# Kernel tuning notes

Measured on AMD Instinct MI355X. Metric: run time of the kernel, lower is better.

Reference implementation:

```python
import jax, jax.numpy as jnp
import numpy as np

VOCAB, HIDDEN, EMB_DIM = 30522, 768, 128
B, QLEN, DLEN = 1024, 32, 180
NEG = -1e4  # masked doc-token similarity
EPS = 1e-12


def setup_inputs() -> dict:
    key = jax.random.key(0)
    k1, k2, k3, k4, k5, k6 = jax.random.split(key, 6)
    return {
        "query_input_ids": jax.random.randint(k1, (B, QLEN), 0, VOCAB, dtype=jnp.int64) if jax.config.jax_enable_x64 else jax.random.randint(k1, (B, QLEN), 0, VOCAB, dtype=jnp.int32),
        "query_attention_mask": jax.random.randint(k2, (B, QLEN), 0, 2, dtype=jnp.int32),
        "doc_input_ids": jax.random.randint(k3, (B, DLEN), 0, VOCAB, dtype=jnp.int32),
        "doc_attention_mask": jax.random.randint(k4, (B, DLEN), 0, 2, dtype=jnp.int32),
        "embed_table": jax.random.normal(k5, (VOCAB, HIDDEN), dtype=jnp.float32) * 0.02,
        "proj_w": jax.random.normal(k6, (HIDDEN, EMB_DIM), dtype=jnp.float32) * 0.02,
        "proj_b": jnp.zeros((EMB_DIM,), dtype=jnp.float32),
    }


def _encode(ids, embed_table, proj_w, proj_b):
    # token embedding lookup -> linear projection -> L2 normalize (ColBERT-style)
    h = embed_table[ids]                      # (B, L, HIDDEN)
    e = jnp.einsum('blh,hd->bld', h, proj_w) + proj_b  # (B, L, EMB_DIM)
    e = e / (jnp.linalg.norm(e, axis=-1, keepdims=True) + EPS)
    return e


def reference(query_input_ids, query_attention_mask, doc_input_ids,
              doc_attention_mask, embed_table, proj_w, proj_b):
    q = _encode(query_input_ids, embed_table, proj_w, proj_b)  # (B, Q, D)
    d = _encode(doc_input_ids, embed_table, proj_w, proj_b)    # (B, T, D)
    # Batched MaxSim: sim[b,q,t] = <q_emb, d_emb>
    sim = jnp.einsum('bqd,btd->bqt', q, d)
    sim = jnp.where(doc_attention_mask[:, None, :] > 0, sim, NEG)
    max_sim = sim.max(axis=-1)                                  # (B, Q)
    scores = (max_sim * query_attention_mask.astype(max_sim.dtype)).sum(axis=-1)
    return scores  # (B,)
```

## Files before the change

kernel.cpp:

```cpp
#include <hip/hip_runtime.h>
#include <math.h>

#define VOCAB  30522
#define HIDDEN 768
#define EMB    128
#define BATCH  1024
#define QLEN   32
#define DLEN   180
#define NEGV   (-1e4f)

typedef __attribute__((ext_vector_type(8))) short bf16x8;
typedef __attribute__((ext_vector_type(4))) float f32x4;

__device__ __forceinline__ unsigned short f2bf(float x) {
  union { float f; unsigned u; } v; v.f = x;
  unsigned r = v.u + 0x7FFFu + ((v.u >> 16) & 1u);
  return (unsigned short)(r >> 16);
}
__device__ __forceinline__ float bf2f(unsigned short h) {
  union { float f; unsigned u; } v; v.u = ((unsigned)h) << 16;
  return v.f;
}

__global__ __launch_bounds__(256) void prep_wt(
    const float* __restrict__ W, unsigned short* __restrict__ wth,
    unsigned short* __restrict__ wtl) {
  __shared__ float tile[32][33];
  const int k0 = blockIdx.x * 32, n0 = blockIdx.y * 32;
  const int t = threadIdx.x, r = t >> 5, c = t & 31;
#pragma unroll
  for (int i = 0; i < 4; ++i) {
    int kr = r + i * 8;
    tile[kr][c] = W[(size_t)(k0 + kr) * EMB + n0 + c];
  }
  __syncthreads();
#pragma unroll
  for (int i = 0; i < 4; ++i) {
    int nr = r + i * 8;
    float x = tile[c][nr];
    unsigned short hi = f2bf(x);
    unsigned short lo = f2bf(x - bf2f(hi));
    wth[(size_t)(n0 + nr) * HIDDEN + k0 + c] = hi;
    wtl[(size_t)(n0 + nr) * HIDDEN + k0 + c] = lo;
  }
}

__global__ __launch_bounds__(256) void colbert_proj_mfma(
    const float* __restrict__ emb, const unsigned short* __restrict__ wth,
    const unsigned short* __restrict__ wtl, const float* __restrict__ bias,
    unsigned short* __restrict__ pebf) {
  __shared__ __align__(16) char smem[55296];
  unsigned short* Ah = (unsigned short*)smem;
  unsigned short* Al = Ah + 64 * 72;
  unsigned short* Wh = Al + 64 * 72;
  unsigned short* Wl = Wh + 128 * 72;

  const int tid  = threadIdx.x;
  const int lane = tid & 63;
  const int wid  = tid >> 6;
  const int wm   = wid & 1;
  const int wn   = wid >> 1;
  const int lr   = lane & 15;
  const int kq   = lane >> 4;
  const int row0 = blockIdx.x * 64;

  f32x4 acc[2][4];
#pragma unroll
  for (int mi = 0; mi < 2; ++mi)
#pragma unroll
    for (int ni = 0; ni < 4; ++ni) acc[mi][ni] = (f32x4)0.f;

  for (int hc = 0; hc < HIDDEN / 64; ++hc) {
    __syncthreads();
#pragma unroll
    for (int i = 0; i < 4; ++i) {
      int idx = i * 256 + tid;
      int row = idx >> 4, c4 = idx & 15;
      int gr = row0 + row; if (gr > VOCAB - 1) gr = VOCAB - 1;
      float4 v = *(const float4*)(emb + (size_t)gr * HIDDEN + hc * 64 + c4 * 4);
      float xs[4] = {v.x, v.y, v.z, v.w};
      ushort4 hh, ll;
      unsigned short* hp = (unsigned short*)&hh;
      unsigned short* lp = (unsigned short*)&ll;
#pragma unroll
      for (int j = 0; j < 4; ++j) {
        hp[j] = f2bf(xs[j]);
        lp[j] = f2bf(xs[j] - bf2f(hp[j]));
      }
      *(ushort4*)&Ah[row * 72 + c4 * 4] = hh;
      *(ushort4*)&Al[row * 72 + c4 * 4] = ll;
    }
#pragma unroll
    for (int i = 0; i < 4; ++i) {
      int idx = i * 256 + tid;
      int n = idx >> 3, k8 = idx & 7;
      size_t src = (size_t)n * HIDDEN + hc * 64 + k8 * 8;
      *(uint4*)&Wh[n * 72 + k8 * 8] = *(const uint4*)(wth + src);
      *(uint4*)&Wl[n * 72 + k8 * 8] = *(const uint4*)(wtl + src);
    }
    __syncthreads();

#pragma unroll
    for (int kk = 0; kk < 2; ++kk) {
      const int ko = kk * 32 + kq * 8;
      bf16x8 ah[2], al[2], bh[4], bl[4];
#pragma unroll
      for (int mi = 0; mi < 2; ++mi) {
        int r = wm * 32 + mi * 16 + lr;
        ah[mi] = *(bf16x8*)&Ah[r * 72 + ko];
        al[mi] = *(bf16x8*)&Al[r * 72 + ko];
      }
#pragma unroll
      for (int ni = 0; ni < 4; ++ni) {
        int n = wn * 64 + ni * 16 + lr;
        bh[ni] = *(bf16x8*)&Wh[n * 72 + ko];
        bl[ni] = *(bf16x8*)&Wl[n * 72 + ko];
      }
#pragma unroll
      for (int mi = 0; mi < 2; ++mi)
#pragma unroll
        for (int ni = 0; ni < 4; ++ni) {
          acc[mi][ni] = __builtin_amdgcn_mfma_f32_16x16x32_bf16(ah[mi], bh[ni], acc[mi][ni], 0, 0, 0);
          acc[mi][ni] = __builtin_amdgcn_mfma_f32_16x16x32_bf16(ah[mi], bl[ni], acc[mi][ni], 0, 0, 0);
          acc[mi][ni] = __builtin_amdgcn_mfma_f32_16x16x32_bf16(al[mi], bh[ni], acc[mi][ni], 0, 0, 0);
        }
    }
  }

  __syncthreads();
  float* ep = (float*)smem;
#pragma unroll
  for (int ni = 0; ni < 4; ++ni) {
    int col = wn * 64 + ni * 16 + lr;
    float bb = bias[col];
#pragma unroll
    for (int mi = 0; mi < 2; ++mi)
#pragma unroll
      for (int j = 0; j < 4; ++j) {
        int r = wm * 32 + mi * 16 + kq * 4 + j;
        ep[r * 132 + col] = acc[mi][ni][j] + bb;
      }
  }
  __syncthreads();
  {
    int row = tid >> 2, quad = tid & 3;
    float4 vv[8];
    float ss = 0.f;
#pragma unroll
    for (int i = 0; i < 8; ++i) {
      vv[i] = *(float4*)&ep[row * 132 + quad * 32 + i * 4];
      ss += vv[i].x * vv[i].x + vv[i].y * vv[i].y + vv[i].z * vv[i].z + vv[i].w * vv[i].w;
    }
    ss += __shfl_xor(ss, 1);
    ss += __shfl_xor(ss, 2);
    float sc = 1.f / (sqrtf(ss) + 1e-12f);
    int gr = row0 + row;
    if (gr < VOCAB) {
#pragma unroll
      for (int i = 0; i < 8; ++i) {
        ushort4 o;
        o.x = f2bf(vv[i].x * sc); o.y = f2bf(vv[i].y * sc);
        o.z = f2bf(vv[i].z * sc); o.w = f2bf(vv[i].w * sc);
        *(ushort4*)&pebf[(size_t)gr * EMB + quad * 32 + i * 4] = o;
      }
    }
  }
}

__global__ __launch_bounds__(256) void colbert_score_mfma(
    const int* __restrict__ qids, const int* __restrict__ qmask,
    const int* __restrict__ dids, const int* __restrict__ dmask,
    const unsigned short* __restrict__ pebf, float* __restrict__ out) {
  __shared__ int sqid[32];
  __shared__ int sdid[192];
  __shared__ unsigned char smsk[192];
  __shared__ float wmax[4][32];

  const int b    = blockIdx.x;
  const int tid  = threadIdx.x;
  const int lane = tid & 63;
  const int wid  = tid >> 6;
  const int lr   = lane & 15;
  const int kq   = lane >> 4;

  if (tid < 32) sqid[tid] = qids[b * QLEN + tid];
  if (tid < 192) {
    if (tid < DLEN) {
      sdid[tid] = dids[b * DLEN + tid];
      smsk[tid] = (unsigned char)(dmask[b * DLEN + tid] > 0 ? 1 : 0);
    } else {
      sdid[tid] = 0;
      smsk[tid] = 0;
    }
  }
  __syncthreads();

  bf16x8 af[2][4];
#pragma unroll
  for (int mi = 0; mi < 2; ++mi) {
    size_t base = (size_t)sqid[mi * 16 + lr] * EMB + kq * 8;
#pragma unroll
    for (int ks = 0; ks < 4; ++ks)
      af[mi][ks] = *(const bf16x8*)(pebf + base + ks * 32);
  }
  const int n0 = wid * 48;
  bf16x8 bf[3][4];
#pragma unroll
  for (int ni = 0; ni < 3; ++ni) {
    size_t base = (size_t)sdid[n0 + ni * 16 + lr] * EMB + kq * 8;
#pragma unroll
    for (int ks = 0; ks < 4; ++ks)
      bf[ni][ks] = *(const bf16x8*)(pebf + base + ks * 32);
  }

  f32x4 acc[2][3];
#pragma unroll
  for (int mi = 0; mi < 2; ++mi)
#pragma unroll
    for (int ni = 0; ni < 3; ++ni) acc[mi][ni] = (f32x4)0.f;

#pragma unroll
  for (int ks = 0; ks < 4; ++ks)
#pragma unroll
    for (int mi = 0; mi < 2; ++mi)
#pragma unroll
      for (int ni = 0; ni < 3; ++ni)
        acc[mi][ni] = __builtin_amdgcn_mfma_f32_16x16x32_bf16(af[mi][ks], bf[ni][ks], acc[mi][ni], 0, 0, 0);

#pragma unroll
  for (int mi = 0; mi < 2; ++mi) {
#pragma unroll
    for (int j = 0; j < 4; ++j) {
      float m = -3.0e38f;
#pragma unroll
      for (int ni = 0; ni < 3; ++ni) {
        int t = n0 + ni * 16 + lr;
        float s = smsk[t] ? acc[mi][ni][j] : NEGV;
        m = fmaxf(m, s);
      }
#pragma unroll
      for (int x = 1; x < 16; x <<= 1) m = fmaxf(m, __shfl_xor(m, x));
      if (lr == 0) wmax[wid][mi * 16 + kq * 4 + j] = m;
    }
  }
  __syncthreads();

  if (tid < 32) {
    float m = fmaxf(fmaxf(wmax[0][tid], wmax[1][tid]),
                    fmaxf(wmax[2][tid], wmax[3][tid]));
    float s = m * (float)qmask[b * QLEN + tid];
#pragma unroll
    for (int x = 1; x < 32; x <<= 1) s += __shfl_xor(s, x);
    if (tid == 0) out[b] = s;
  }
}

extern "C" void kernel_launch(void* const* d_in, const int* in_sizes, int n_in,
                              void* d_out, int out_size, void* d_ws, size_t ws_size,
                              hipStream_t stream) {
  const int*   qids  = (const int*)d_in[0];
  const int*   qmask = (const int*)d_in[1];
  const int*   dids  = (const int*)d_in[2];
  const int*   dmask = (const int*)d_in[3];
  const float* emb   = (const float*)d_in[4];
  const float* W     = (const float*)d_in[5];
  const float* bias  = (const float*)d_in[6];
  float*       out   = (float*)d_out;

  char* ws = (char*)d_ws;
  unsigned short* pebf = (unsigned short*)ws;
  unsigned short* wth  = (unsigned short*)(ws + 7813632);
  unsigned short* wtl  = (unsigned short*)(ws + 7813632 + 196608);

  prep_wt<<<dim3(HIDDEN / 32, EMB / 32), 256, 0, stream>>>(W, wth, wtl);
  colbert_proj_mfma<<<(VOCAB + 63) / 64, 256, 0, stream>>>(emb, wth, wtl, bias, pebf);
  colbert_score_mfma<<<BATCH, 256, 0, stream>>>(qids, qmask, dids, dmask, pebf, out);
}
```

Before: 51.03 us.

## Prepack W into MFMA fragment layout and double-buffer swizzled A tiles

The weight prep kernel now writes hi/lo bf16 splits of W directly in per-lane MFMA fragment order, so the projection kernel loads B operands straight from global or L2 with no LDS staging. The embedding A tile is prefetched into registers for the next chunk while the current one is consumed from a double-buffered, XOR-swizzled LDS buffer, which leaves one barrier per chunk. The bf16 hi/lo split now uses the packed v_cvt_pk_bf16_f32 instruction. This cuts LDS traffic and synchronisation and overlaps global loads with MFMA work, at the cost of more register pressure and B fragments read from global memory by every block.

```diff
diff --git a/kernel.cpp b/kernel.cpp
--- a/kernel.cpp
+++ b/kernel.cpp
@@ -21,39 +21,45 @@
   union { float f; unsigned u; } v; v.u = ((unsigned)h) << 16;
   return v.f;
 }
-
-__global__ __launch_bounds__(256) void prep_wt(
-    const float* __restrict__ W, unsigned short* __restrict__ wth,
-    unsigned short* __restrict__ wtl) {
-  __shared__ float tile[32][33];
-  const int k0 = blockIdx.x * 32, n0 = blockIdx.y * 32;
-  const int t = threadIdx.x, r = t >> 5, c = t & 31;
-#pragma unroll
-  for (int i = 0; i < 4; ++i) {
-    int kr = r + i * 8;
-    tile[kr][c] = W[(size_t)(k0 + kr) * EMB + n0 + c];
-  }
-  __syncthreads();
-#pragma unroll
-  for (int i = 0; i < 4; ++i) {
-    int nr = r + i * 8;
-    float x = tile[c][nr];
+__device__ __forceinline__ void split_pk(float x0, float x1, unsigned& h, unsigned& l) {
+  asm("v_cvt_pk_bf16_f32 %0, %1, %2" : "=v"(h) : "v"(x0), "v"(x1));
+  float h0, h1;
+  h0 = __uint_as_float(h << 16);
+  h1 = __uint_as_float(h & 0xffff0000u);
+  float l0 = x0 - h0, l1 = x1 - h1;
+  asm("v_cvt_pk_bf16_f32 %0, %1, %2" : "=v"(l) : "v"(l0), "v"(l1));
+}
+
+__global__ __launch_bounds__(256) void prep_wfrag(
+    const float* __restrict__ W, unsigned short* __restrict__ wfh,
+    unsigned short* __restrict__ wfl) {
+  int g = blockIdx.x * 256 + threadIdx.x;
+  if (g >= 24 * 8 * 64) return;
+  int lane = g & 63, nt = (g >> 6) & 7, kk = g >> 9;
+  int lr = lane & 15, kq = lane >> 4;
+  int n = nt * 16 + lr;
+  int k0 = kk * 32 + kq * 8;
+  unsigned short hh[8], ll[8];
+#pragma unroll
+  for (int j = 0; j < 8; ++j) {
+    float x = W[(size_t)(k0 + j) * EMB + n];
     unsigned short hi = f2bf(x);
-    unsigned short lo = f2bf(x - bf2f(hi));
-    wth[(size_t)(n0 + nr) * HIDDEN + k0 + c] = hi;
-    wtl[(size_t)(n0 + nr) * HIDDEN + k0 + c] = lo;
+    hh[j] = hi;
+    ll[j] = f2bf(x - bf2f(hi));
+  }
+  size_t base = (size_t)g * 8;
+#pragma unroll
+  for (int j = 0; j < 2; ++j) {
+    *(ushort4*)(wfh + base + j * 4) = *(ushort4*)(hh + j * 4);
+    *(ushort4*)(wfl + base + j * 4) = *(ushort4*)(ll + j * 4);
   }
 }
 
 __global__ __launch_bounds__(256) void colbert_proj_mfma(
-    const float* __restrict__ emb, const unsigned short* __restrict__ wth,
-    const unsigned short* __restrict__ wtl, const float* __restrict__ bias,
+    const float* __restrict__ emb, const unsigned short* __restrict__ wfh,
+    const unsigned short* __restrict__ wfl, const float* __restrict__ bias,
     unsigned short* __restrict__ pebf) {
-  __shared__ __align__(16) char smem[55296];
-  unsigned short* Ah = (unsigned short*)smem;
-  unsigned short* Al = Ah + 64 * 72;
-  unsigned short* Wh = Al + 64 * 72;
-  unsigned short* Wl = Wh + 128 * 72;
+  __shared__ __align__(16) char smem[34816];
 
   const int tid  = threadIdx.x;
   const int lane = tid & 63;
@@ -64,57 +70,70 @@
   const int kq   = lane >> 4;
   const int row0 = blockIdx.x * 64;
 
+  const int srow = tid >> 4;
+  const int sc4  = tid & 15;
+
   f32x4 acc[2][4];
 #pragma unroll
   for (int mi = 0; mi < 2; ++mi)
 #pragma unroll
     for (int ni = 0; ni < 4; ++ni) acc[mi][ni] = (f32x4)0.f;
 
-  for (int hc = 0; hc < HIDDEN / 64; ++hc) {
-    __syncthreads();
-#pragma unroll
-    for (int i = 0; i < 4; ++i) {
-      int idx = i * 256 + tid;
-      int row = idx >> 4, c4 = idx & 15;
-      int gr = row0 + row; if (gr > VOCAB - 1) gr = VOCAB - 1;
-      float4 v = *(const float4*)(emb + (size_t)gr * HIDDEN + hc * 64 + c4 * 4);
-      float xs[4] = {v.x, v.y, v.z, v.w};
-      ushort4 hh, ll;
-      unsigned short* hp = (unsigned short*)&hh;
-      unsigned short* lp = (unsigned short*)&ll;
-#pragma unroll
-      for (int j = 0; j < 4; ++j) {
-        hp[j] = f2bf(xs[j]);
-        lp[j] = f2bf(xs[j] - bf2f(hp[j]));
-      }
-      *(ushort4*)&Ah[row * 72 + c4 * 4] = hh;
-      *(ushort4*)&Al[row * 72 + c4 * 4] = ll;
-    }
-#pragma unroll
-    for (int i = 0; i < 4; ++i) {
-      int idx = i * 256 + tid;
-      int n = idx >> 3, k8 = idx & 7;
-      size_t src = (size_t)n * HIDDEN + hc * 64 + k8 * 8;
-      *(uint4*)&Wh[n * 72 + k8 * 8] = *(const uint4*)(wth + src);
-      *(uint4*)&Wl[n * 72 + k8 * 8] = *(const uint4*)(wtl + src);
-    }
-    __syncthreads();
-
+  float4 ar[4];
+#pragma unroll
+  for (int i = 0; i < 4; ++i) {
+    int row = i * 16 + srow;
+    int gr = row0 + row; if (gr > VOCAB - 1) gr = VOCAB - 1;
+    ar[i] = *(const float4*)(emb + (size_t)gr * HIDDEN + sc4 * 4);
+  }
+
+#define WRITE_A(bufidx)                                                        \
+  {                                                                            \
+    char* Ahb = smem + (bufidx) * 16384;                                       \
+    char* Alb = Ahb + 8192;                                                    \
+    _Pragma("unroll")                                                          \
+    for (int i = 0; i < 4; ++i) {                                              \
+      int row = i * 16 + srow;                                                 \
+      unsigned h0, l0, h1, l1;                                                 \
+      split_pk(ar[i].x, ar[i].y, h0, l0);                                      \
+      split_pk(ar[i].z, ar[i].w, h1, l1);                                      \
+      int byt = (row * 128 + sc4 * 8) ^ ((row & 7) << 4);                      \
+      *(uint2*)(Ahb + byt) = make_uint2(h0, h1);                               \
+      *(uint2*)(Alb + byt) = make_uint2(l0, l1);                               \
+    }                                                                          \
+  }
+
+  WRITE_A(0);
+  __syncthreads();
+
+  for (int hc = 0; hc < 12; ++hc) {
+    const int cur = hc & 1;
+    if (hc < 11) {
+#pragma unroll
+      for (int i = 0; i < 4; ++i) {
+        int row = i * 16 + srow;
+        int gr = row0 + row; if (gr > VOCAB - 1) gr = VOCAB - 1;
+        ar[i] = *(const float4*)(emb + (size_t)gr * HIDDEN + (hc + 1) * 64 + sc4 * 4);
+      }
+    }
+    char* Ahb = smem + cur * 16384;
+    char* Alb = Ahb + 8192;
 #pragma unroll
     for (int kk = 0; kk < 2; ++kk) {
-      const int ko = kk * 32 + kq * 8;
-      bf16x8 ah[2], al[2], bh[4], bl[4];
+      bf16x8 bh[4], bl[4];
+      size_t bbase = ((size_t)((hc * 2 + kk) * 8 + wn * 4) * 64 + lane) * 8;
+#pragma unroll
+      for (int ni = 0; ni < 4; ++ni) {
+        bh[ni] = *(const bf16x8*)(wfh + bbase + ni * 512);
+        bl[ni] = *(const bf16x8*)(wfl + bbase + ni * 512);
+      }
+      bf16x8 ah[2], al[2];
 #pragma unroll
       for (int mi = 0; mi < 2; ++mi) {
-        int r = wm * 32 + mi * 16 + lr;
-        ah[mi] = *(bf16x8*)&Ah[r * 72 + ko];
-        al[mi] = *(bf16x8*)&Al[r * 72 + ko];
-      }
-#pragma unroll
-      for (int ni = 0; ni < 4; ++ni) {
-        int n = wn * 64 + ni * 16 + lr;
-        bh[ni] = *(bf16x8*)&Wh[n * 72 + ko];
-        bl[ni] = *(bf16x8*)&Wl[n * 72 + ko];
+        int row = wm * 32 + mi * 16 + lr;
+        int byt = (row * 128 + kk * 64 + kq * 16) ^ ((row & 7) << 4);
+        ah[mi] = *(bf16x8*)(Ahb + byt);
+        al[mi] = *(bf16x8*)(Alb + byt);
       }
 #pragma unroll
       for (int mi = 0; mi < 2; ++mi)
@@ -125,9 +144,10 @@
           acc[mi][ni] = __builtin_amdgcn_mfma_f32_16x16x32_bf16(al[mi], bh[ni], acc[mi][ni], 0, 0, 0);
         }
     }
-  }
-
-  __syncthreads();
+    if (hc < 11) WRITE_A(cur ^ 1);
+    __syncthreads();
+  }
+
   float* ep = (float*)smem;
 #pragma unroll
   for (int ni = 0; ni < 4; ++ni) {
@@ -269,10 +289,10 @@
 
   char* ws = (char*)d_ws;
   unsigned short* pebf = (unsigned short*)ws;
-  unsigned short* wth  = (unsigned short*)(ws + 7813632);
-  unsigned short* wtl  = (unsigned short*)(ws + 7813632 + 196608);
-
-  prep_wt<<<dim3(HIDDEN / 32, EMB / 32), 256, 0, stream>>>(W, wth, wtl);
-  colbert_proj_mfma<<<(VOCAB + 63) / 64, 256, 0, stream>>>(emb, wth, wtl, bias, pebf);
+  unsigned short* wfh  = (unsigned short*)(ws + 7813632);
+  unsigned short* wfl  = (unsigned short*)(ws + 7813632 + 196608);
+
+  prep_wfrag<<<48, 256, 0, stream>>>(W, wfh, wfl);
+  colbert_proj_mfma<<<(VOCAB + 63) / 64, 256, 0, stream>>>(emb, wfh, wfl, bias, pebf);
   colbert_score_mfma<<<BATCH, 256, 0, stream>>>(qids, qmask, dids, dmask, pebf, out);
 }
```

After: 48.96 us. 4.1% less time.
